# Kernel optimization log

Hardware: AMD Instinct MI355X
Metric: run time of the kernel (lower is better)

Reference implementation:

```python
import jax, jax.numpy as jnp
import numpy as np

B, N, E, D, H, M = 64, 4096, 8192, 256, 256, 64


def setup_inputs() -> dict:
    key = jax.random.key(0)
    ks = jax.random.split(key, 12)
    s = lambda fan_in: 1.0 / np.sqrt(fan_in)
    return {
        "node_embeddings": jax.random.normal(ks[0], (B, N, D), jnp.float32),
        "army_counts": jax.random.randint(ks[1], (B, N), 0, 50).astype(jnp.float32),
        "action_edges": jax.random.randint(ks[2], (B, E, 2), 0, N, dtype=jnp.int32),
        # edge_scorer: Linear(2H, H) -> ReLU -> Linear(H, 1)
        "W1": jax.random.normal(ks[3], (2 * H, H), jnp.float32) * s(2 * H),
        "b1": jnp.zeros((H,), jnp.float32),
        "W2": jax.random.normal(ks[4], (H, 1), jnp.float32) * s(H),
        "b2": jnp.zeros((1,), jnp.float32),
        # army_scorer: Linear(2D, 128) -> ReLU -> Linear(128, M)
        "A1": jax.random.normal(ks[5], (2 * D, 128), jnp.float32) * s(2 * D),
        "a1": jnp.zeros((128,), jnp.float32),
        "A2": jax.random.normal(ks[6], (128, M), jnp.float32) * s(128.0),
        "a2": jnp.zeros((M,), jnp.float32),
    }


def reference(node_embeddings, army_counts, W1, b1, W2, b2, A1, a1, A2, a2, action_edges):
    # node_embeddings: [B, N, D]; action_edges: [B, E, 2]; army_counts: [B, N]
    b, n, d = node_embeddings.shape
    m = A2.shape[1]
    dt = node_embeddings.dtype

    src = action_edges[..., 0]  # [B, E]
    tgt = action_edges[..., 1]
    src_c = jnp.clip(src, 0, n - 1)
    tgt_c = jnp.clip(tgt, 0, n - 1)

    # Gather endpoint embeddings: [B, E, D]
    src_e = jnp.take_along_axis(node_embeddings, src_c[..., None], axis=1)
    tgt_e = jnp.take_along_axis(node_embeddings, tgt_c[..., None], axis=1)
    edge_embed = jnp.concatenate([src_e, tgt_e], axis=-1)  # [B, E, 2D]

    # edge scorer MLP -> [B, E]
    h = jax.nn.relu(edge_embed @ W1 + b1)
    edge_logits = (h @ W2 + b2)[..., 0]

    # army scorer MLP -> [B, E, M]
    g = jax.nn.relu(edge_embed @ A1 + a1)
    army_logits = g @ A2 + a2

    src_armies = jnp.take_along_axis(army_counts, src_c, axis=1)  # [B, E]
    tgt_armies = jnp.take_along_axis(army_counts, tgt_c, axis=1)

    valid_edges = (src >= 0) & (tgt >= 0)
    bad_edges = valid_edges & ((src_armies <= 2) | (tgt_armies >= 3 * src_armies))
    edge_logits = edge_logits - bad_edges.astype(dt) * 1.0

    invalid_self = (src == tgt) & valid_edges
    edge_logits = edge_logits - invalid_self.astype(dt) * 100.0

    max_sendable = src_armies - 1  # [B, E]
    army_range = jnp.arange(m, dtype=dt)[None, None, :]  # [1, 1, M]
    valid_mask = army_range <= max_sendable[..., None]
    army_logits = jnp.where(valid_mask, army_logits, jnp.asarray(-1e9, dt))

    return edge_logits, army_logits
```

## Files before the change

kernel.cpp:

```cpp
#include <hip/hip_runtime.h>

#define BB   64
#define NN   4096
#define EE   8192
#define DD   256
#define HH   256
#define MM   64
#define K1   512
#define NC   384
#define TE   64
#define BLOCK 512
#define KC   32
#define NCHUNK 16
#define ASTR 40
#define GSTR 136
#define ABUF 2560
#define BE_TOT (BB * EE)
#define WCTF_ELEMS (NC * K1)
#define A2F_ELEMS  (128 * MM)
#define WS_NEEDED ((size_t)(WCTF_ELEMS + A2F_ELEMS) * sizeof(short))

typedef float f32x4 __attribute__((ext_vector_type(4)));
typedef short bf16x8 __attribute__((ext_vector_type(8)));

__device__ __forceinline__ short f2bf(float f) {
    unsigned u = __float_as_uint(f);
    unsigned r = (u + 0x7fffu + ((u >> 16) & 1u)) >> 16;
    return (short)r;
}

__global__ void AttackHead_prep(const float* __restrict__ W1,
                                const float* __restrict__ A1,
                                const float* __restrict__ A2,
                                short* __restrict__ wctf,
                                short* __restrict__ a2f) {
    int t = blockIdx.x * 256 + threadIdx.x;
    if (t < 131072) {
        int k = t >> 8, n = t & 255;
        int c = k >> 5, kr = k & 31, quad = kr >> 3, j = kr & 7;
        int nt = n >> 4, l15 = n & 15;
        wctf[((c * 24 + nt) * 64 + quad * 16 + l15) * 8 + j] = f2bf(W1[t]);
    } else if (t < 131072 + 65536) {
        int t2 = t - 131072;
        int k = t2 >> 7, n = 256 + (t2 & 127);
        int c = k >> 5, kr = k & 31, quad = kr >> 3, j = kr & 7;
        int nt = n >> 4, l15 = n & 15;
        wctf[((c * 24 + nt) * 64 + quad * 16 + l15) * 8 + j] = f2bf(A1[t2]);
    } else if (t < 131072 + 65536 + 8192) {
        int t3 = t - 131072 - 65536;
        int k = t3 >> 6, n = t3 & 63;
        int ks = k >> 5, kr = k & 31, quad = kr >> 3, j = kr & 7;
        int nt2 = n >> 4, l15 = n & 15;
        a2f[((ks * 4 + nt2) * 64 + quad * 16 + l15) * 8 + j] = f2bf(A2[t3]);
    }
}

template <bool USE_WS>
__device__ __forceinline__ bf16x8 load_bfrag(const short* __restrict__ wf,
                                             const float* __restrict__ W1,
                                             const float* __restrict__ A1,
                                             int c, int nt, int lane) {
    if (USE_WS) {
        return *(const bf16x8*)(wf + ((c * 24 + nt) * 64 + lane) * 8);
    } else {
        int l15 = lane & 15, quad = lane >> 4;
        int n = nt * 16 + l15;
        bf16x8 r;
        #pragma unroll
        for (int j = 0; j < 8; ++j) {
            int k = c * KC + quad * 8 + j;
            float v = (n < HH) ? W1[k * HH + n] : A1[k * 128 + (n - HH)];
            r[j] = f2bf(v);
        }
        return r;
    }
}

template <bool USE_WS>
__device__ __forceinline__ bf16x8 load_a2frag(const short* __restrict__ a2f,
                                              const float* __restrict__ A2,
                                              int ks, int nt2, int lane) {
    if (USE_WS) {
        return *(const bf16x8*)(a2f + ((ks * 4 + nt2) * 64 + lane) * 8);
    } else {
        int l15 = lane & 15, quad = lane >> 4;
        int n = nt2 * 16 + l15;
        bf16x8 r;
        #pragma unroll
        for (int j = 0; j < 8; ++j) {
            int k = ks * 32 + quad * 8 + j;
            r[j] = f2bf(A2[k * MM + n]);
        }
        return r;
    }
}

template <bool USE_WS>
__global__ __launch_bounds__(BLOCK, 4)
void AttackHead_main(const float* __restrict__ nodes,
                     const float* __restrict__ army,
                     const int* __restrict__ edges,
                     const float* __restrict__ W1,
                     const float* __restrict__ b1,
                     const float* __restrict__ W2,
                     const float* __restrict__ b2,
                     const float* __restrict__ A1,
                     const float* __restrict__ a1,
                     const float* __restrict__ A2,
                     const float* __restrict__ a2,
                     const short* __restrict__ wctf,
                     const short* __restrict__ a2f,
                     float* __restrict__ out) {
    __shared__ __align__(16) short smem[8704];
    __shared__ int   srcn[TE], tgtn[TE];
    __shared__ float elog[TE], maxs[TE];

    const int tid = threadIdx.x;
    const int bb  = blockIdx.x;
    const int bglob = bb >> 7;
    const long be0 = (long)bb * TE;

    if (tid < TE) {
        long be = be0 + tid;
        int src = edges[2 * be], tgt = edges[2 * be + 1];
        int sc = min(max(src, 0), NN - 1);
        int tc = min(max(tgt, 0), NN - 1);
        srcn[tid] = sc; tgtn[tid] = tc;
        float sa = army[(size_t)bglob * NN + sc];
        float ta = army[(size_t)bglob * NN + tc];
        bool valid = (src >= 0) && (tgt >= 0);
        bool bad   = valid && (sa <= 2.0f || ta >= 3.0f * sa);
        bool selfe = valid && (src == tgt);
        elog[tid] = b2[0] - (bad ? 1.0f : 0.0f) - (selfe ? 100.0f : 0.0f);
        maxs[tid] = sa - 1.0f;
    }
    __syncthreads();

    const int w    = tid >> 6;
    const int lane = tid & 63;
    const int quad = lane >> 4;
    const int l15  = lane & 15;

    const int srow = tid >> 3;
    const int sj   = tid & 7;
    const size_t nbase_g = (size_t)bglob * NN;

    f32x4 acc[4][3] = {};

    {
        int node = srcn[srow];
        float4 v = *(const float4*)(nodes + (nbase_g + node) * DD + sj * 4);
        short4 s;
        s.x = f2bf(v.x); s.y = f2bf(v.y); s.z = f2bf(v.z); s.w = f2bf(v.w);
        *(short4*)(&smem[0 * ABUF + srow * ASTR + sj * 4]) = s;
    }
    float4 lda = *(const float4*)(nodes + (nbase_g + srcn[srow]) * DD + KC + sj * 4);

    int bufc = 0;
    for (int c = 0; c < NCHUNK; ++c) {
        __syncthreads();

        float4 ldn;
        if (c + 2 < NCHUNK) {
            int cc = c + 2;
            int node = (cc < 8) ? srcn[srow] : tgtn[srow];
            ldn = *(const float4*)(nodes + (nbase_g + node) * DD + (cc & 7) * KC + sj * 4);
        }

        bf16x8 bf0 = load_bfrag<USE_WS>(wctf, W1, A1, c, w * 3 + 0, lane);
        bf16x8 bf1 = load_bfrag<USE_WS>(wctf, W1, A1, c, w * 3 + 1, lane);
        bf16x8 bf2 = load_bfrag<USE_WS>(wctf, W1, A1, c, w * 3 + 2, lane);

        const short* Ab = &smem[bufc * ABUF];
        bf16x8 af[4];
        #pragma unroll
        for (int mt = 0; mt < 4; ++mt)
            af[mt] = *(const bf16x8*)(&Ab[(mt * 16 + l15) * ASTR + quad * 8]);

        #pragma unroll
        for (int mt = 0; mt < 4; ++mt) {
            acc[mt][0] = __builtin_amdgcn_mfma_f32_16x16x32_bf16(af[mt], bf0, acc[mt][0], 0, 0, 0);
            acc[mt][1] = __builtin_amdgcn_mfma_f32_16x16x32_bf16(af[mt], bf1, acc[mt][1], 0, 0, 0);
            acc[mt][2] = __builtin_amdgcn_mfma_f32_16x16x32_bf16(af[mt], bf2, acc[mt][2], 0, 0, 0);
        }

        int bufw = (bufc + 1 == 3) ? 0 : bufc + 1;
        if (c + 1 < NCHUNK) {
            short4 s;
            s.x = f2bf(lda.x); s.y = f2bf(lda.y); s.z = f2bf(lda.z); s.w = f2bf(lda.w);
            *(short4*)(&smem[bufw * ABUF + srow * ASTR + sj * 4]) = s;
            lda = ldn;
        }
        bufc = bufw;
    }

    __syncthreads();

    short* Gs = smem;
    float ep[4][4] = {};
    #pragma unroll
    for (int jn = 0; jn < 3; ++jn) {
        int ct = (w * 3 + jn) * 16 + l15;
        float bias = (ct < HH) ? b1[ct] : a1[ct - HH];
        if (ct < HH) {
            float w2v = W2[ct];
            #pragma unroll
            for (int mt = 0; mt < 4; ++mt)
                #pragma unroll
                for (int r = 0; r < 4; ++r) {
                    float h = fmaxf(acc[mt][jn][r] + bias, 0.0f);
                    ep[mt][r] += h * w2v;
                }
        } else {
            int gc = ct - HH;
            #pragma unroll
            for (int mt = 0; mt < 4; ++mt)
                #pragma unroll
                for (int r = 0; r < 4; ++r) {
                    float g = fmaxf(acc[mt][jn][r] + bias, 0.0f);
                    Gs[(mt * 16 + quad * 4 + r) * GSTR + gc] = f2bf(g);
                }
        }
    }
    if (w < 6) {
        #pragma unroll
        for (int msk = 1; msk <= 8; msk <<= 1)
            #pragma unroll
            for (int mt = 0; mt < 4; ++mt)
                #pragma unroll
                for (int r = 0; r < 4; ++r)
                    ep[mt][r] += __shfl_xor(ep[mt][r], msk, 64);
        if (l15 == 0) {
            #pragma unroll
            for (int mt = 0; mt < 4; ++mt)
                #pragma unroll
                for (int r = 0; r < 4; ++r)
                    atomicAdd(&elog[mt * 16 + quad * 4 + r], ep[mt][r]);
        }
    }
    __syncthreads();

    const int mt2 = w >> 1;
    const int nh  = w & 1;
    f32x4 acc2[2] = {};
    #pragma unroll
    for (int ks = 0; ks < 4; ++ks) {
        bf16x8 ga = *(const bf16x8*)(&Gs[(mt2 * 16 + l15) * GSTR + ks * 32 + quad * 8]);
        #pragma unroll
        for (int nb = 0; nb < 2; ++nb) {
            bf16x8 bv = load_a2frag<USE_WS>(a2f, A2, ks, nh * 2 + nb, lane);
            acc2[nb] = __builtin_amdgcn_mfma_f32_16x16x32_bf16(ga, bv, acc2[nb], 0, 0, 0);
        }
    }

    if (tid < TE) out[be0 + tid] = elog[tid];

    #pragma unroll
    for (int nb = 0; nb < 2; ++nb) {
        int col = (nh * 2 + nb) * 16 + l15;
        float a2v = a2[col];
        #pragma unroll
        for (int r = 0; r < 4; ++r) {
            int grow = mt2 * 16 + quad * 4 + r;
            float val = acc2[nb][r] + a2v;
            if ((float)col > maxs[grow]) val = -1e9f;
            out[(size_t)BE_TOT + (size_t)(be0 + grow) * MM + col] = val;
        }
    }
}

extern "C" void kernel_launch(void* const* d_in, const int* in_sizes, int n_in,
                              void* d_out, int out_size, void* d_ws, size_t ws_size,
                              hipStream_t stream) {
    const float* nodes = (const float*)d_in[0];
    const float* army  = (const float*)d_in[1];
    const int*   edges = (const int*)d_in[2];
    const float* W1    = (const float*)d_in[3];
    const float* b1    = (const float*)d_in[4];
    const float* W2    = (const float*)d_in[5];
    const float* b2    = (const float*)d_in[6];
    const float* A1    = (const float*)d_in[7];
    const float* a1    = (const float*)d_in[8];
    const float* A2    = (const float*)d_in[9];
    const float* a2    = (const float*)d_in[10];
    float* out = (float*)d_out;

    int nblocks = BE_TOT / TE;

    if (ws_size >= WS_NEEDED) {
        short* wctf = (short*)d_ws;
        short* a2f  = wctf + WCTF_ELEMS;
        AttackHead_prep<<<800, 256, 0, stream>>>(W1, A1, A2, wctf, a2f);
        AttackHead_main<true><<<nblocks, BLOCK, 0, stream>>>(
            nodes, army, edges, W1, b1, W2, b2, A1, a1, A2, a2, wctf, a2f, out);
    } else {
        AttackHead_main<false><<<nblocks, BLOCK, 0, stream>>>(
            nodes, army, edges, W1, b1, W2, b2, A1, a1, A2, a2,
            (const short*)nullptr, (const short*)nullptr, out);
    }
}
```

Before: 685.5 us.

## Halve edge tile, widen K chunk, remap blocks, use packed bf16 convert

Each block now handles 32 edges instead of 64, using 64-wide K chunks with a double-buffered LDS staging area instead of a triple buffer. The launch bound rises to 8 blocks per CU, and block indices are swizzled so consecutive blocks spread across graphs. The conversion uses a packed v_cvt_pk_bf16_f32 instruction, and barriers use an explicit lgkmcnt wait. Smaller tiles mean more blocks and more occupancy, but the weight fragments are reused across fewer edges, so weight load traffic per edge doubles.

```diff
diff --git a/kernel.cpp b/kernel.cpp
--- a/kernel.cpp
+++ b/kernel.cpp
@@ -8,14 +8,16 @@
 #define MM   64
 #define K1   512
 #define NC   384
-#define TE   64
+#define TE   32
 #define BLOCK 512
-#define KC   32
-#define NCHUNK 16
-#define ASTR 40
+#define KC   64
+#define NCHUNK 8
+#define ASTR 88
 #define GSTR 136
-#define ABUF 2560
+#define ABUF (TE * ASTR)
+#define SMEM_SHORTS (2 * ABUF)
 #define BE_TOT (BB * EE)
+#define NBLK (BE_TOT / TE)
 #define WCTF_ELEMS (NC * K1)
 #define A2F_ELEMS  (128 * MM)
 #define WS_NEEDED ((size_t)(WCTF_ELEMS + A2F_ELEMS) * sizeof(short))
@@ -27,6 +29,14 @@
     unsigned u = __float_as_uint(f);
     unsigned r = (u + 0x7fffu + ((u >> 16) & 1u)) >> 16;
     return (short)r;
+}
+__device__ __forceinline__ int cvt_pk_bf16(float lo, float hi) {
+    int r;
+    asm("v_cvt_pk_bf16_f32 %0, %1, %2" : "=v"(r) : "v"(lo), "v"(hi));
+    return r;
+}
+__device__ __forceinline__ void barrier_lgkm() {
+    asm volatile("s_waitcnt lgkmcnt(0)\n\ts_barrier" ::: "memory");
 }
 
 __global__ void AttackHead_prep(const float* __restrict__ W1,
@@ -68,7 +78,7 @@
         bf16x8 r;
         #pragma unroll
         for (int j = 0; j < 8; ++j) {
-            int k = c * KC + quad * 8 + j;
+            int k = c * 32 + quad * 8 + j;
             float v = (n < HH) ? W1[k * HH + n] : A1[k * 128 + (n - HH)];
             r[j] = f2bf(v);
         }
@@ -96,7 +106,7 @@
 }
 
 template <bool USE_WS>
-__global__ __launch_bounds__(BLOCK, 4)
+__global__ __launch_bounds__(BLOCK, 8)
 void AttackHead_main(const float* __restrict__ nodes,
                      const float* __restrict__ army,
                      const int* __restrict__ edges,
@@ -111,13 +121,13 @@
                      const short* __restrict__ wctf,
                      const short* __restrict__ a2f,
                      float* __restrict__ out) {
-    __shared__ __align__(16) short smem[8704];
+    __shared__ __align__(16) short smem[SMEM_SHORTS];
     __shared__ int   srcn[TE], tgtn[TE];
     __shared__ float elog[TE], maxs[TE];
 
     const int tid = threadIdx.x;
-    const int bb  = blockIdx.x;
-    const int bglob = bb >> 7;
+    const int bb  = ((blockIdx.x & 7) << 11) | (blockIdx.x >> 3);
+    const int bglob = bb >> 8;
     const long be0 = (long)bb * TE;
 
     if (tid < TE) {
@@ -141,63 +151,58 @@
     const int quad = lane >> 4;
     const int l15  = lane & 15;
 
-    const int srow = tid >> 3;
-    const int sj   = tid & 7;
+    const int srow = tid >> 4;
+    const int sj   = tid & 15;
     const size_t nbase_g = (size_t)bglob * NN;
-
-    f32x4 acc[4][3] = {};
+    const float* srcp = nodes + (nbase_g + (size_t)srcn[srow]) * DD + sj * 4;
+    const float* tgtp = nodes + (nbase_g + (size_t)tgtn[srow]) * DD + sj * 4;
+
+    f32x4 acc[2][3] = {};
 
     {
-        int node = srcn[srow];
-        float4 v = *(const float4*)(nodes + (nbase_g + node) * DD + sj * 4);
-        short4 s;
-        s.x = f2bf(v.x); s.y = f2bf(v.y); s.z = f2bf(v.z); s.w = f2bf(v.w);
-        *(short4*)(&smem[0 * ABUF + srow * ASTR + sj * 4]) = s;
-    }
-    float4 lda = *(const float4*)(nodes + (nbase_g + srcn[srow]) * DD + KC + sj * 4);
-
-    int bufc = 0;
+        float4 v = *(const float4*)(srcp);
+        int2 s;
+        s.x = cvt_pk_bf16(v.x, v.y); s.y = cvt_pk_bf16(v.z, v.w);
+        *(int2*)(&smem[srow * ASTR + sj * 4]) = s;
+    }
+    float4 lda = *(const float4*)(srcp + 64);
+
+    #pragma unroll
     for (int c = 0; c < NCHUNK; ++c) {
-        __syncthreads();
+        barrier_lgkm();
 
         float4 ldn;
-        if (c + 2 < NCHUNK) {
-            int cc = c + 2;
-            int node = (cc < 8) ? srcn[srow] : tgtn[srow];
-            ldn = *(const float4*)(nodes + (nbase_g + node) * DD + (cc & 7) * KC + sj * 4);
-        }
-
-        bf16x8 bf0 = load_bfrag<USE_WS>(wctf, W1, A1, c, w * 3 + 0, lane);
-        bf16x8 bf1 = load_bfrag<USE_WS>(wctf, W1, A1, c, w * 3 + 1, lane);
-        bf16x8 bf2 = load_bfrag<USE_WS>(wctf, W1, A1, c, w * 3 + 2, lane);
-
-        const short* Ab = &smem[bufc * ABUF];
-        bf16x8 af[4];
-        #pragma unroll
-        for (int mt = 0; mt < 4; ++mt)
-            af[mt] = *(const bf16x8*)(&Ab[(mt * 16 + l15) * ASTR + quad * 8]);
-
-        #pragma unroll
-        for (int mt = 0; mt < 4; ++mt) {
-            acc[mt][0] = __builtin_amdgcn_mfma_f32_16x16x32_bf16(af[mt], bf0, acc[mt][0], 0, 0, 0);
-            acc[mt][1] = __builtin_amdgcn_mfma_f32_16x16x32_bf16(af[mt], bf1, acc[mt][1], 0, 0, 0);
-            acc[mt][2] = __builtin_amdgcn_mfma_f32_16x16x32_bf16(af[mt], bf2, acc[mt][2], 0, 0, 0);
-        }
-
-        int bufw = (bufc + 1 == 3) ? 0 : bufc + 1;
+        if (c + 2 < NCHUNK)
+            ldn = *(const float4*)((((c + 2) < 4) ? srcp : tgtp) + ((c + 2) & 3) * 64);
+
+        const short* Ab = &smem[(c & 1) * ABUF];
+        #pragma unroll
+        for (int kk = 0; kk < 2; ++kk) {
+            bf16x8 b0 = load_bfrag<USE_WS>(wctf, W1, A1, 2 * c + kk, w * 3 + 0, lane);
+            bf16x8 b1f = load_bfrag<USE_WS>(wctf, W1, A1, 2 * c + kk, w * 3 + 1, lane);
+            bf16x8 b2f = load_bfrag<USE_WS>(wctf, W1, A1, 2 * c + kk, w * 3 + 2, lane);
+            bf16x8 a0 = *(const bf16x8*)(&Ab[(0 * 16 + l15) * ASTR + kk * 32 + quad * 8]);
+            bf16x8 a1f = *(const bf16x8*)(&Ab[(1 * 16 + l15) * ASTR + kk * 32 + quad * 8]);
+            acc[0][0] = __builtin_amdgcn_mfma_f32_16x16x32_bf16(a0, b0, acc[0][0], 0, 0, 0);
+            acc[0][1] = __builtin_amdgcn_mfma_f32_16x16x32_bf16(a0, b1f, acc[0][1], 0, 0, 0);
+            acc[0][2] = __builtin_amdgcn_mfma_f32_16x16x32_bf16(a0, b2f, acc[0][2], 0, 0, 0);
+            acc[1][0] = __builtin_amdgcn_mfma_f32_16x16x32_bf16(a1f, b0, acc[1][0], 0, 0, 0);
+            acc[1][1] = __builtin_amdgcn_mfma_f32_16x16x32_bf16(a1f, b1f, acc[1][1], 0, 0, 0);
+            acc[1][2] = __builtin_amdgcn_mfma_f32_16x16x32_bf16(a1f, b2f, acc[1][2], 0, 0, 0);
+        }
+
         if (c + 1 < NCHUNK) {
-            short4 s;
-            s.x = f2bf(lda.x); s.y = f2bf(lda.y); s.z = f2bf(lda.z); s.w = f2bf(lda.w);
-            *(short4*)(&smem[bufw * ABUF + srow * ASTR + sj * 4]) = s;
-            lda = ldn;
-        }
-        bufc = bufw;
+            int2 s;
+            s.x = cvt_pk_bf16(lda.x, lda.y); s.y = cvt_pk_bf16(lda.z, lda.w);
+            *(int2*)(&smem[((c + 1) & 1) * ABUF + srow * ASTR + sj * 4]) = s;
+        }
+        if (c + 2 < NCHUNK) lda = ldn;
     }
 
     __syncthreads();
 
     short* Gs = smem;
-    float ep[4][4] = {};
+    float ep[2][4] = {};
     #pragma unroll
     for (int jn = 0; jn < 3; ++jn) {
         int ct = (w * 3 + jn) * 16 + l15;
@@ -205,7 +210,7 @@
         if (ct < HH) {
             float w2v = W2[ct];
             #pragma unroll
-            for (int mt = 0; mt < 4; ++mt)
+            for (int mt = 0; mt < 2; ++mt)
                 #pragma unroll
                 for (int r = 0; r < 4; ++r) {
                     float h = fmaxf(acc[mt][jn][r] + bias, 0.0f);
@@ -214,7 +219,7 @@
         } else {
             int gc = ct - HH;
             #pragma unroll
-            for (int mt = 0; mt < 4; ++mt)
+            for (int mt = 0; mt < 2; ++mt)
                 #pragma unroll
                 for (int r = 0; r < 4; ++r) {
                     float g = fmaxf(acc[mt][jn][r] + bias, 0.0f);
@@ -226,13 +231,13 @@
         #pragma unroll
         for (int msk = 1; msk <= 8; msk <<= 1)
             #pragma unroll
-            for (int mt = 0; mt < 4; ++mt)
+            for (int mt = 0; mt < 2; ++mt)
                 #pragma unroll
                 for (int r = 0; r < 4; ++r)
                     ep[mt][r] += __shfl_xor(ep[mt][r], msk, 64);
         if (l15 == 0) {
             #pragma unroll
-            for (int mt = 0; mt < 4; ++mt)
+            for (int mt = 0; mt < 2; ++mt)
                 #pragma unroll
                 for (int r = 0; r < 4; ++r)
                     atomicAdd(&elog[mt * 16 + quad * 4 + r], ep[mt][r]);
@@ -240,29 +245,25 @@
     }
     __syncthreads();
 
-    const int mt2 = w >> 1;
-    const int nh  = w & 1;
-    f32x4 acc2[2] = {};
+    const int mt2 = w >> 2;
+    const int nt2 = w & 3;
+    f32x4 acc2 = {};
     #pragma unroll
     for (int ks = 0; ks < 4; ++ks) {
         bf16x8 ga = *(const bf16x8*)(&Gs[(mt2 * 16 + l15) * GSTR + ks * 32 + quad * 8]);
-        #pragma unroll
-        for (int nb = 0; nb < 2; ++nb) {
-            bf16x8 bv = load_a2frag<USE_WS>(a2f, A2, ks, nh * 2 + nb, lane);
-            acc2[nb] = __builtin_amdgcn_mfma_f32_16x16x32_bf16(ga, bv, acc2[nb], 0, 0, 0);
-        }
+        bf16x8 bv = load_a2frag<USE_WS>(a2f, A2, ks, nt2, lane);
+        acc2 = __builtin_amdgcn_mfma_f32_16x16x32_bf16(ga, bv, acc2, 0, 0, 0);
     }
 
     if (tid < TE) out[be0 + tid] = elog[tid];
 
-    #pragma unroll
-    for (int nb = 0; nb < 2; ++nb) {
-        int col = (nh * 2 + nb) * 16 + l15;
+    {
+        int col = nt2 * 16 + l15;
         float a2v = a2[col];
         #pragma unroll
         for (int r = 0; r < 4; ++r) {
             int grow = mt2 * 16 + quad * 4 + r;
-            float val = acc2[nb][r] + a2v;
+            float val = acc2[r] + a2v;
             if ((float)col > maxs[grow]) val = -1e9f;
             out[(size_t)BE_TOT + (size_t)(be0 + grow) * MM + col] = val;
         }
@@ -285,16 +286,14 @@
     const float* a2    = (const float*)d_in[10];
     float* out = (float*)d_out;
 
-    int nblocks = BE_TOT / TE;
-
     if (ws_size >= WS_NEEDED) {
         short* wctf = (short*)d_ws;
         short* a2f  = wctf + WCTF_ELEMS;
         AttackHead_prep<<<800, 256, 0, stream>>>(W1, A1, A2, wctf, a2f);
-        AttackHead_main<true><<<nblocks, BLOCK, 0, stream>>>(
+        AttackHead_main<true><<<NBLK, BLOCK, 0, stream>>>(
             nodes, army, edges, W1, b1, W2, b2, A1, a1, A2, a2, wctf, a2f, out);
     } else {
-        AttackHead_main<false><<<nblocks, BLOCK, 0, stream>>>(
+        AttackHead_main<false><<<NBLK, BLOCK, 0, stream>>>(
             nodes, army, edges, W1, b1, W2, b2, A1, a1, A2, a2,
             (const short*)nullptr, (const short*)nullptr, out);
     }
```

Result: slower. 710.8 us (+3.7%).
